# Kernel tuning notes

Measured on AMD Instinct MI355X. Metric: run time of the kernel, lower is better.

The kernel has to match this reference:

```python
import jax, jax.numpy as jnp
import numpy as np

EMBED_DIM = 1024
WINDOW = 256
NUM_HEADS = 16
HEAD_DIM = EMBED_DIM // NUM_HEADS
SCALE = HEAD_DIM ** (-0.5)


def setup_inputs() -> dict:
    key = jax.random.key(0)
    ks = jax.random.split(key, 9)
    B, S, E = 4, 4096, EMBED_DIM
    std = E ** (-0.5)
    x = jax.random.normal(ks[0], (B, S, E), dtype=jnp.float32)
    Wq = jax.random.normal(ks[1], (E, E), dtype=jnp.float32) * std
    Wk = jax.random.normal(ks[2], (E, E), dtype=jnp.float32) * std
    Wv = jax.random.normal(ks[3], (E, E), dtype=jnp.float32) * std
    Wo = jax.random.normal(ks[4], (E, E), dtype=jnp.float32) * std
    bq = jax.random.normal(ks[5], (E,), dtype=jnp.float32) * 0.01
    bk = jax.random.normal(ks[6], (E,), dtype=jnp.float32) * 0.01
    bv = jax.random.normal(ks[7], (E,), dtype=jnp.float32) * 0.01
    bo = jax.random.normal(ks[8], (E,), dtype=jnp.float32) * 0.01
    return {"x": x, "Wq": Wq, "bq": bq, "Wk": Wk, "bk": bk,
            "Wv": Wv, "bv": bv, "Wo": Wo, "bo": bo}


def reference(x, Wq, bq, Wk, bk, Wv, bv, Wo, bo):
    B, S, E = x.shape
    W = WINDOW
    nw = S // W  # seq_len chosen divisible by window_size
    # projections (torch Linear: x @ W.T + b); no head split in the original
    q = x @ Wq.T + bq
    k = x @ Wk.T + bk
    v = x @ Wv.T + bv
    # split into non-overlapping windows: [B, nw, W, E]
    qw = q.reshape(B, nw, W, E)
    kw = k.reshape(B, nw, W, E)
    vw = v.reshape(B, nw, W, E)
    scores = jnp.einsum('bnqe,bnke->bnqk', qw, kw) * SCALE  # [B, nw, W, W]
    causal = jnp.tril(jnp.ones((W, W), dtype=bool))
    scores = jnp.where(causal, scores, -jnp.inf)
    attn = jax.nn.softmax(scores, axis=-1)
    out = jnp.einsum('bnqk,bnke->bnqe', attn, vw).reshape(B, S, E)
    out = out @ Wo.T + bo
    return out + x
```

## Files before the change

kernel.cpp:

```cpp
#include <hip/hip_runtime.h>
#include <hip/hip_bf16.h>


typedef unsigned short u16;
typedef __attribute__((ext_vector_type(8))) short short8;
typedef __attribute__((ext_vector_type(4))) float f32x4;

__device__ __forceinline__ u16 f2bf(float f) {
    __hip_bfloat16 h = __float2bfloat16(f);
    return __builtin_bit_cast(u16, h);
}

__global__ void cast_x(const float* __restrict__ x, u16* __restrict__ xb, u16* __restrict__ xt) {
    __shared__ float lt[64][65];
    const int t = threadIdx.x;
    const int e0 = blockIdx.x * 64, i0 = blockIdx.y * 64;
    const int tr = t >> 3, tc = (t & 7) * 8;
#pragma unroll
    for (int p = 0; p < 2; ++p) {
        int r = p * 32 + tr;
        const float* s = x + (size_t)(i0 + r) * 1024 + e0 + tc;
        float4 a = *(const float4*)s, b = *(const float4*)(s + 4);
        short8 o;
        o[0] = (short)f2bf(a.x); o[1] = (short)f2bf(a.y); o[2] = (short)f2bf(a.z); o[3] = (short)f2bf(a.w);
        o[4] = (short)f2bf(b.x); o[5] = (short)f2bf(b.y); o[6] = (short)f2bf(b.z); o[7] = (short)f2bf(b.w);
        *(short8*)(xb + (size_t)(i0 + r) * 1024 + e0 + tc) = o;
        lt[r][tc + 0] = a.x; lt[r][tc + 1] = a.y; lt[r][tc + 2] = a.z; lt[r][tc + 3] = a.w;
        lt[r][tc + 4] = b.x; lt[r][tc + 5] = b.y; lt[r][tc + 6] = b.z; lt[r][tc + 7] = b.w;
    }
    __syncthreads();
#pragma unroll
    for (int p = 0; p < 2; ++p) {
        int r = p * 32 + tr;
        short8 o;
#pragma unroll
        for (int j = 0; j < 8; ++j) o[j] = (short)f2bf(lt[tc + j][r]);
        *(short8*)(xt + (size_t)(e0 + r) * 16384 + i0 + tc) = o;
    }
}

__global__ void wcast(const float* __restrict__ Wq, const float* __restrict__ Wk,
                      const float* __restrict__ Wv, const float* __restrict__ Wo,
                      u16* __restrict__ WqT, u16* __restrict__ WkT,
                      u16* __restrict__ WvT, u16* __restrict__ Wob)
{
    __shared__ float lt[64][65];
    const int which = blockIdx.x >> 8;
    const int bid = blockIdx.x & 255;
    const int c0 = (bid & 15) * 64, r0 = (bid >> 4) * 64;
    const int t = threadIdx.x;
    const int tr = t >> 3, tc = (t & 7) * 8;
    const float* src = which == 0 ? Wq : which == 1 ? Wk : which == 2 ? Wv : Wo;
    if (which == 3) {
#pragma unroll
        for (int p = 0; p < 2; ++p) {
            int r = p * 32 + tr;
            const float* s = src + (size_t)(r0 + r) * 1024 + c0 + tc;
            float4 a = *(const float4*)s, b = *(const float4*)(s + 4);
            short8 o;
            o[0] = (short)f2bf(a.x); o[1] = (short)f2bf(a.y); o[2] = (short)f2bf(a.z); o[3] = (short)f2bf(a.w);
            o[4] = (short)f2bf(b.x); o[5] = (short)f2bf(b.y); o[6] = (short)f2bf(b.z); o[7] = (short)f2bf(b.w);
            *(short8*)(Wob + (size_t)(r0 + r) * 1024 + c0 + tc) = o;
        }
        return;
    }
    u16* dst = which == 0 ? WqT : which == 1 ? WkT : WvT;
#pragma unroll
    for (int p = 0; p < 2; ++p) {
        int r = p * 32 + tr;
        const float* s = src + (size_t)(r0 + r) * 1024 + c0 + tc;
        float4 a = *(const float4*)s, b = *(const float4*)(s + 4);
        lt[r][tc + 0] = a.x; lt[r][tc + 1] = a.y; lt[r][tc + 2] = a.z; lt[r][tc + 3] = a.w;
        lt[r][tc + 4] = b.x; lt[r][tc + 5] = b.y; lt[r][tc + 6] = b.z; lt[r][tc + 7] = b.w;
    }
    __syncthreads();
#pragma unroll
    for (int p = 0; p < 2; ++p) {
        int r = p * 32 + tr;
        short8 o;
#pragma unroll
        for (int j = 0; j < 8; ++j) o[j] = (short)f2bf(lt[tc + j][r]);
        *(short8*)(dst + (size_t)(c0 + r) * 1024 + r0 + tc) = o;
    }
}

__global__ void ub2(const float* __restrict__ Wk, const float* __restrict__ bq,
                    const float* __restrict__ Wo, const float* __restrict__ bv,
                    const float* __restrict__ bo, float* __restrict__ u, float* __restrict__ b2)
{
    const int t = threadIdx.x, bid = blockIdx.x;
    if (bid < 4) {
        int b = bid * 256 + t;
        float acc = 0.f;
        for (int o = 0; o < 1024; ++o) acc += Wk[(size_t)o * 1024 + b] * bq[o];
        u[b] = acc;
    } else {
        int n = (bid - 4) * 16 + (t >> 4);
        int l = t & 15;
        float acc = 0.f;
        for (int m = l; m < 1024; m += 16) acc += Wo[(size_t)n * 1024 + m] * bv[m];
#pragma unroll
        for (int s = 1; s < 16; s <<= 1) acc += __shfl_xor(acc, s, 64);
        if (l == 0) b2[n] = acc + bo[n];
    }
}

__global__ __launch_bounds__(256, 4) void gemm_small_dual(
    const u16* __restrict__ HA, const u16* __restrict__ HB, u16* __restrict__ HC,
    const u16* __restrict__ WA, const u16* __restrict__ WB, u16* __restrict__ WC)
{
    __shared__ __align__(16) u16 At[64 * 64], Bt[64 * 64];
    const bool sec = blockIdx.x >= 256;
    const u16* A = sec ? WA : HA;
    const u16* B = sec ? WB : HB;
    u16* C = sec ? WC : HC;
    const int bid = blockIdx.x & 255;
    const int m0 = (bid >> 4) * 64, n0 = (bid & 15) * 64;
    const int t = threadIdx.x, lane = t & 63, w = t >> 6;
    const int l15 = lane & 15, lk = lane >> 4;

    f32x4 acc[4];
#pragma unroll
    for (int m = 0; m < 4; ++m) acc[m] = (f32x4){0.f, 0.f, 0.f, 0.f};

    for (int k0 = 0; k0 < 1024; k0 += 64) {
        __syncthreads();
#pragma unroll
        for (int p = 0; p < 2; ++p) {
            int e = p * 2048 + t * 8;
            int row = e >> 6, col = e & 63;
            short8 va = *(const short8*)(A + (size_t)(m0 + row) * 1024 + k0 + col);
            *(short8*)((char*)At + row * 128 + ((col * 2) ^ ((row & 7) << 4))) = va;
            short8 vb = *(const short8*)(B + (size_t)(n0 + row) * 1024 + k0 + col);
            *(short8*)((char*)Bt + row * 128 + ((col * 2) ^ ((row & 7) << 4))) = vb;
        }
        __syncthreads();
#pragma unroll
        for (int ks = 0; ks < 2; ++ks) {
            int bc = ks * 64 + lk * 16;
            int brow = w * 16 + l15;
            short8 bfr = *(const short8*)((char*)Bt + brow * 128 + (bc ^ ((brow & 7) << 4)));
#pragma unroll
            for (int m = 0; m < 4; ++m) {
                int arow = m * 16 + l15;
                short8 af = *(const short8*)((char*)At + arow * 128 + (bc ^ ((arow & 7) << 4)));
                acc[m] = __builtin_amdgcn_mfma_f32_16x16x32_bf16(af, bfr, acc[m], 0, 0, 0);
            }
        }
    }
#pragma unroll
    for (int m = 0; m < 4; ++m)
#pragma unroll
        for (int r = 0; r < 4; ++r) {
            int row = m0 + m * 16 + lk * 4 + r;
            int col = n0 + w * 16 + l15;
            C[(size_t)row * 1024 + col] = f2bf(acc[m][r]);
        }
}

template <int EPI>
__global__ __launch_bounds__(256, 2) void gemm_bt(
    const u16* __restrict__ A, const u16* __restrict__ B,
    int M, int N, int K,
    const float* __restrict__ bias0,
    u16* __restrict__ Cb, float* __restrict__ Cf, const float* __restrict__ resid)
{
    __shared__ __align__(16) u16 At[128 * 64];
    __shared__ __align__(16) u16 Bt[128 * 64];
    const int t = threadIdx.x;
    const int lane = t & 63;
    const int wid = t >> 6;
    const int wm = wid >> 1, wn = wid & 1;
    const int l15 = lane & 15, lk = lane >> 4;

    const int bid = blockIdx.y * gridDim.x + blockIdx.x;
    const int nwg = gridDim.x * gridDim.y;
    const int cpx = nwg >> 3;
    const int swz = (bid & 7) * cpx + (bid >> 3);
    const int tn = swz & 7;
    const int tm = swz >> 3;
    const int m0 = tm * 128, n0 = tn * 128;

    f32x4 acc[4][4];
#pragma unroll
    for (int m = 0; m < 4; ++m)
#pragma unroll
        for (int n = 0; n < 4; ++n)
            acc[m][n] = (f32x4){0.f, 0.f, 0.f, 0.f};

    for (int k0 = 0; k0 < K; k0 += 64) {
        __syncthreads();
#pragma unroll
        for (int p = 0; p < 4; ++p) {
            int e = p * 2048 + t * 8;
            int row = e >> 6, col = e & 63;
            short8 va = *(const short8*)(A + (size_t)(m0 + row) * K + k0 + col);
            *(short8*)((char*)At + row * 128 + ((col * 2) ^ ((row & 7) << 4))) = va;
            short8 vb = *(const short8*)(B + (size_t)(n0 + row) * K + k0 + col);
            *(short8*)((char*)Bt + row * 128 + ((col * 2) ^ ((row & 7) << 4))) = vb;
        }
        __syncthreads();
#pragma unroll
        for (int ks = 0; ks < 2; ++ks) {
            const int bc = ks * 64 + lk * 16;
            short8 af[4], bfr[4];
#pragma unroll
            for (int m = 0; m < 4; ++m) {
                int row = wm * 64 + m * 16 + l15;
                af[m] = *(const short8*)((char*)At + row * 128 + (bc ^ ((row & 7) << 4)));
            }
#pragma unroll
            for (int n = 0; n < 4; ++n) {
                int row = wn * 64 + n * 16 + l15;
                bfr[n] = *(const short8*)((char*)Bt + row * 128 + (bc ^ ((row & 7) << 4)));
            }
#pragma unroll
            for (int m = 0; m < 4; ++m)
#pragma unroll
                for (int n = 0; n < 4; ++n)
                    acc[m][n] = __builtin_amdgcn_mfma_f32_16x16x32_bf16(af[m], bfr[n], acc[m][n], 0, 0, 0);
        }
    }

#pragma unroll
    for (int m = 0; m < 4; ++m) {
#pragma unroll
        for (int n = 0; n < 4; ++n) {
            int col = n0 + wn * 64 + n * 16 + l15;
            float bv = bias0[col];
#pragma unroll
            for (int r = 0; r < 4; ++r) {
                int row = m0 + wm * 64 + m * 16 + lk * 4 + r;
                float v = acc[m][n][r] + bv;
                if (EPI == 0)
                    Cb[(size_t)row * N + col] = f2bf(v);
                else
                    Cf[(size_t)row * N + col] = v + resid[(size_t)row * N + col];
            }
        }
    }
}

__global__ __launch_bounds__(256, 1) void attn_win(
    const u16* __restrict__ y, const u16* __restrict__ xb,
    const u16* __restrict__ xt, u16* __restrict__ z)
{
    __shared__ __align__(16) char smem[100608];
    float* S = (float*)smem;
    u16* P = (u16*)(smem + 65792);
    float* rmax = (float*)(smem + 98560);
    float* rsum = (float*)(smem + 99584);
    u16* Qt = (u16*)smem;
    u16* Kt = (u16*)(smem + 8192);
    u16* Vl = (u16*)smem;

    const int t = threadIdx.x;
    const int lane = t & 63, wv = t >> 6;
    const int l15 = lane & 15, lk = lane >> 4;
    const int bid = blockIdx.x;
    const int swz = (bid & 7) * 32 + (bid >> 3);
    const int win = swz >> 2, qc = swz & 3;
    const size_t qrow0 = (size_t)win * 256 + qc * 64;
    const size_t krow0 = (size_t)win * 256;

    f32x4 acc[4][4];
#pragma unroll
    for (int m = 0; m < 4; ++m)
#pragma unroll
        for (int n = 0; n < 4; ++n)
            acc[m][n] = (f32x4){0.f, 0.f, 0.f, 0.f};

    for (int e0 = 0; e0 < 1024; e0 += 64) {
        __syncthreads();
#pragma unroll
        for (int p = 0; p < 2; ++p) {
            int e = p * 2048 + t * 8;
            int row = e >> 6, col = e & 63;
            short8 v = *(const short8*)(y + (qrow0 + row) * 1024 + e0 + col);
            *(short8*)((char*)Qt + row * 128 + ((col * 2) ^ ((row & 7) << 4))) = v;
        }
#pragma unroll
        for (int p = 0; p < 8; ++p) {
            int e = p * 2048 + t * 8;
            int row = e >> 6, col = e & 63;
            short8 v = *(const short8*)(xb + (krow0 + row) * 1024 + e0 + col);
            *(short8*)((char*)Kt + row * 128 + ((col * 2) ^ ((row & 7) << 4))) = v;
        }
        __syncthreads();
#pragma unroll
        for (int ks = 0; ks < 2; ++ks) {
            const int bc = ks * 64 + lk * 16;
            short8 af[4], bfr[4];
#pragma unroll
            for (int m = 0; m < 4; ++m) {
                int row = m * 16 + l15;
                af[m] = *(const short8*)((char*)Qt + row * 128 + (bc ^ ((row & 7) << 4)));
            }
#pragma unroll
            for (int n = 0; n < 4; ++n) {
                int row = wv * 64 + n * 16 + l15;
                bfr[n] = *(const short8*)((char*)Kt + row * 128 + (bc ^ ((row & 7) << 4)));
            }
#pragma unroll
            for (int m = 0; m < 4; ++m)
#pragma unroll
                for (int n = 0; n < 4; ++n)
                    acc[m][n] = __builtin_amdgcn_mfma_f32_16x16x32_bf16(af[m], bfr[n], acc[m][n], 0, 0, 0);
        }
    }
    __syncthreads();

#pragma unroll
    for (int m = 0; m < 4; ++m) {
#pragma unroll
        for (int n = 0; n < 4; ++n) {
            int col = wv * 64 + n * 16 + l15;
#pragma unroll
            for (int r = 0; r < 4; ++r) {
                int row = m * 16 + lk * 4 + r;
                int qpos = qc * 64 + row;
                float v = acc[m][n][r] * 0.125f;
                S[row * 257 + col] = (col <= qpos) ? v : -1e30f;
            }
        }
    }
    __syncthreads();
    {
        const int row = t & 63, q4 = t >> 6;
        float* Sr = S + row * 257 + q4 * 64;
        float lmax = -1e30f;
        for (int i = 0; i < 64; ++i) lmax = fmaxf(lmax, Sr[i]);
        rmax[row * 4 + q4] = lmax;
        __syncthreads();
        float m4 = fmaxf(fmaxf(rmax[row * 4], rmax[row * 4 + 1]),
                         fmaxf(rmax[row * 4 + 2], rmax[row * 4 + 3]));
        float lsum = 0.f;
        for (int i = 0; i < 64; ++i) {
            float e = __expf(Sr[i] - m4);
            Sr[i] = e;
            lsum += e;
        }
        rsum[row * 4 + q4] = lsum;
        __syncthreads();
        float inv = 1.f / (rsum[row * 4] + rsum[row * 4 + 1] + rsum[row * 4 + 2] + rsum[row * 4 + 3]);
#pragma unroll
        for (int i8 = 0; i8 < 8; ++i8) {
            short8 pv;
#pragma unroll
            for (int j = 0; j < 8; ++j) pv[j] = (short)f2bf(Sr[i8 * 8 + j] * inv);
            int col = q4 * 64 + i8 * 8;
            *(short8*)((char*)P + row * 512 + ((col * 2) ^ ((row & 7) << 4))) = pv;
        }
    }

    for (int n0 = 0; n0 < 1024; n0 += 64) {
        __syncthreads();
#pragma unroll
        for (int p = 0; p < 8; ++p) {
            int e = p * 2048 + t * 8;
            int row = e >> 8, col = e & 255;
            short8 v = *(const short8*)(xt + (size_t)(n0 + row) * 16384 + win * 256 + col);
            *(short8*)((char*)Vl + row * 512 + ((col * 2) ^ ((row & 7) << 4))) = v;
        }
        __syncthreads();
        f32x4 acc2[4];
#pragma unroll
        for (int m = 0; m < 4; ++m) acc2[m] = (f32x4){0.f, 0.f, 0.f, 0.f};
#pragma unroll
        for (int ks = 0; ks < 8; ++ks) {
            const int bc = ks * 64 + lk * 16;
            short8 af[4];
#pragma unroll
            for (int m = 0; m < 4; ++m) {
                int row = m * 16 + l15;
                af[m] = *(const short8*)((char*)P + row * 512 + (bc ^ ((row & 7) << 4)));
            }
            int vrow = wv * 16 + l15;
            short8 bfr = *(const short8*)((char*)Vl + vrow * 512 + (bc ^ ((vrow & 7) << 4)));
#pragma unroll
            for (int m = 0; m < 4; ++m)
                acc2[m] = __builtin_amdgcn_mfma_f32_16x16x32_bf16(af[m], bfr, acc2[m], 0, 0, 0);
        }
#pragma unroll
        for (int m = 0; m < 4; ++m) {
#pragma unroll
            for (int r = 0; r < 4; ++r) {
                int row = m * 16 + lk * 4 + r;
                int col = n0 + wv * 16 + l15;
                z[(qrow0 + row) * 1024 + col] = f2bf(acc2[m][r]);
            }
        }
    }
}

extern "C" void kernel_launch(void* const* d_in, const int* in_sizes, int n_in,
                              void* d_out, int out_size, void* d_ws, size_t ws_size,
                              hipStream_t stream) {
    const float* x  = (const float*)d_in[0];
    const float* Wq = (const float*)d_in[1];
    const float* bq = (const float*)d_in[2];
    const float* Wk = (const float*)d_in[3];
    const float* Wv = (const float*)d_in[5];
    const float* bv = (const float*)d_in[6];
    const float* Wo = (const float*)d_in[7];
    const float* bo = (const float*)d_in[8];
    float* out = (float*)d_out;

    char* ws = (char*)d_ws;
    u16* xb  = (u16*)(ws);
    u16* xt  = (u16*)(ws + 33554432);
    u16* yb  = (u16*)(ws + 67108864);
    u16* zb  = (u16*)(ws + 100663296);
    u16* WqT = (u16*)(ws + 134217728);
    u16* WkT = (u16*)(ws + 136314880);
    u16* WvT = (u16*)(ws + 138412032);
    u16* Wob = (u16*)(ws + 140509184);
    u16* Hb  = (u16*)(ws + 142606336);
    u16* W2b = (u16*)(ws + 144703488);
    float* u_  = (float*)(ws + 146800640);
    float* b2_ = (float*)(ws + 146804736);

    cast_x<<<dim3(16, 256), 256, 0, stream>>>(x, xb, xt);
    wcast<<<1024, 256, 0, stream>>>(Wq, Wk, Wv, Wo, WqT, WkT, WvT, Wob);
    ub2<<<68, 256, 0, stream>>>(Wk, bq, Wo, bv, bo, u_, b2_);
    gemm_small_dual<<<512, 256, 0, stream>>>(WkT, WqT, Hb, Wob, WvT, W2b);
    gemm_bt<0><<<dim3(8, 128), 256, 0, stream>>>(xb, Hb, 16384, 1024, 1024, u_, yb, nullptr, nullptr);
    attn_win<<<256, 256, 0, stream>>>(yb, xb, xt, zb);
    gemm_bt<1><<<dim3(8, 128), 256, 0, stream>>>(zb, W2b, 16384, 1024, 1024, b2_, nullptr, out, x);
}
```

Baseline: 221.2 us.

## Register-prefetch GEMM tiles, register-resident softmax, and two blocks per CU for attention

The GEMM now prefetches the next K-tile of A and B into registers while the current tile is computed, which hides global load latency. The attention kernel drops the fp32 S score buffer in shared memory. Softmax now runs on the MFMA accumulators using wave shuffles plus small per-wave max and sum arrays. That cuts shared memory from about 100KB to 75KB, so launch bounds can allow two blocks per CU. s_setprio is also placed around the MFMA bursts, and P is now written with scalar 16-bit stores, which may cost some LDS store efficiency.

```diff
diff --git a/kernel.cpp b/kernel.cpp
--- a/kernel.cpp
+++ b/kernel.cpp
@@ -181,6 +181,8 @@
     const int tm = swz >> 3;
     const int m0 = tm * 128, n0 = tn * 128;
 
+    const int srow = (t * 8) >> 6, scol = (t * 8) & 63;
+
     f32x4 acc[4][4];
 #pragma unroll
     for (int m = 0; m < 4; ++m)
@@ -188,18 +190,29 @@
         for (int n = 0; n < 4; ++n)
             acc[m][n] = (f32x4){0.f, 0.f, 0.f, 0.f};
 
+    short8 pva[4], pvb[4];
+#pragma unroll
+    for (int p = 0; p < 4; ++p) {
+        pva[p] = *(const short8*)(A + (size_t)(m0 + p * 32 + srow) * K + scol);
+        pvb[p] = *(const short8*)(B + (size_t)(n0 + p * 32 + srow) * K + scol);
+    }
+
     for (int k0 = 0; k0 < K; k0 += 64) {
         __syncthreads();
 #pragma unroll
         for (int p = 0; p < 4; ++p) {
-            int e = p * 2048 + t * 8;
-            int row = e >> 6, col = e & 63;
-            short8 va = *(const short8*)(A + (size_t)(m0 + row) * K + k0 + col);
-            *(short8*)((char*)At + row * 128 + ((col * 2) ^ ((row & 7) << 4))) = va;
-            short8 vb = *(const short8*)(B + (size_t)(n0 + row) * K + k0 + col);
-            *(short8*)((char*)Bt + row * 128 + ((col * 2) ^ ((row & 7) << 4))) = vb;
-        }
-        __syncthreads();
+            int row = p * 32 + srow;
+            *(short8*)((char*)At + row * 128 + ((scol * 2) ^ ((row & 7) << 4))) = pva[p];
+            *(short8*)((char*)Bt + row * 128 + ((scol * 2) ^ ((row & 7) << 4))) = pvb[p];
+        }
+        __syncthreads();
+        if (k0 + 64 < K) {
+#pragma unroll
+            for (int p = 0; p < 4; ++p) {
+                pva[p] = *(const short8*)(A + (size_t)(m0 + p * 32 + srow) * K + k0 + 64 + scol);
+                pvb[p] = *(const short8*)(B + (size_t)(n0 + p * 32 + srow) * K + k0 + 64 + scol);
+            }
+        }
 #pragma unroll
         for (int ks = 0; ks < 2; ++ks) {
             const int bc = ks * 64 + lk * 16;
@@ -241,18 +254,17 @@
     }
 }
 
-__global__ __launch_bounds__(256, 1) void attn_win(
+__global__ __launch_bounds__(256, 2) void attn_win(
     const u16* __restrict__ y, const u16* __restrict__ xb,
     const u16* __restrict__ xt, u16* __restrict__ z)
 {
-    __shared__ __align__(16) char smem[100608];
-    float* S = (float*)smem;
-    u16* P = (u16*)(smem + 65792);
-    float* rmax = (float*)(smem + 98560);
-    float* rsum = (float*)(smem + 99584);
+    __shared__ __align__(16) char smem[75776];
     u16* Qt = (u16*)smem;
     u16* Kt = (u16*)(smem + 8192);
     u16* Vl = (u16*)smem;
+    u16* P  = (u16*)(smem + 40960);
+    float* rmax = (float*)(smem + 73728);
+    float* rsum = (float*)(smem + 74752);
 
     const int t = threadIdx.x;
     const int lane = t & 63, wv = t >> 6;
@@ -301,57 +313,73 @@
                 int row = wv * 64 + n * 16 + l15;
                 bfr[n] = *(const short8*)((char*)Kt + row * 128 + (bc ^ ((row & 7) << 4)));
             }
+            __builtin_amdgcn_s_setprio(1);
 #pragma unroll
             for (int m = 0; m < 4; ++m)
 #pragma unroll
                 for (int n = 0; n < 4; ++n)
                     acc[m][n] = __builtin_amdgcn_mfma_f32_16x16x32_bf16(af[m], bfr[n], acc[m][n], 0, 0, 0);
-        }
-    }
-    __syncthreads();
-
-#pragma unroll
-    for (int m = 0; m < 4; ++m) {
+            __builtin_amdgcn_s_setprio(0);
+        }
+    }
+
+#pragma unroll
+    for (int m = 0; m < 4; ++m)
 #pragma unroll
         for (int n = 0; n < 4; ++n) {
             int col = wv * 64 + n * 16 + l15;
 #pragma unroll
             for (int r = 0; r < 4; ++r) {
-                int row = m * 16 + lk * 4 + r;
-                int qpos = qc * 64 + row;
+                int qpos = qc * 64 + m * 16 + lk * 4 + r;
                 float v = acc[m][n][r] * 0.125f;
-                S[row * 257 + col] = (col <= qpos) ? v : -1e30f;
-            }
-        }
-    }
+                acc[m][n][r] = (col <= qpos) ? v : -1e30f;
+            }
+        }
+#pragma unroll
+    for (int m = 0; m < 4; ++m)
+#pragma unroll
+        for (int r = 0; r < 4; ++r) {
+            float tmx = fmaxf(fmaxf(acc[m][0][r], acc[m][1][r]), fmaxf(acc[m][2][r], acc[m][3][r]));
+            tmx = fmaxf(tmx, __shfl_xor(tmx, 1));
+            tmx = fmaxf(tmx, __shfl_xor(tmx, 2));
+            tmx = fmaxf(tmx, __shfl_xor(tmx, 4));
+            tmx = fmaxf(tmx, __shfl_xor(tmx, 8));
+            if (l15 == 0) rmax[(m * 16 + lk * 4 + r) * 4 + wv] = tmx;
+        }
     __syncthreads();
-    {
-        const int row = t & 63, q4 = t >> 6;
-        float* Sr = S + row * 257 + q4 * 64;
-        float lmax = -1e30f;
-        for (int i = 0; i < 64; ++i) lmax = fmaxf(lmax, Sr[i]);
-        rmax[row * 4 + q4] = lmax;
-        __syncthreads();
-        float m4 = fmaxf(fmaxf(rmax[row * 4], rmax[row * 4 + 1]),
-                         fmaxf(rmax[row * 4 + 2], rmax[row * 4 + 3]));
-        float lsum = 0.f;
-        for (int i = 0; i < 64; ++i) {
-            float e = __expf(Sr[i] - m4);
-            Sr[i] = e;
-            lsum += e;
-        }
-        rsum[row * 4 + q4] = lsum;
-        __syncthreads();
-        float inv = 1.f / (rsum[row * 4] + rsum[row * 4 + 1] + rsum[row * 4 + 2] + rsum[row * 4 + 3]);
-#pragma unroll
-        for (int i8 = 0; i8 < 8; ++i8) {
-            short8 pv;
-#pragma unroll
-            for (int j = 0; j < 8; ++j) pv[j] = (short)f2bf(Sr[i8 * 8 + j] * inv);
-            int col = q4 * 64 + i8 * 8;
-            *(short8*)((char*)P + row * 512 + ((col * 2) ^ ((row & 7) << 4))) = pv;
-        }
-    }
+#pragma unroll
+    for (int m = 0; m < 4; ++m)
+#pragma unroll
+        for (int r = 0; r < 4; ++r) {
+            int row = m * 16 + lk * 4 + r;
+            float m4 = fmaxf(fmaxf(rmax[row * 4], rmax[row * 4 + 1]),
+                             fmaxf(rmax[row * 4 + 2], rmax[row * 4 + 3]));
+            float s = 0.f;
+#pragma unroll
+            for (int n = 0; n < 4; ++n) {
+                float e = __expf(acc[m][n][r] - m4);
+                acc[m][n][r] = e;
+                s += e;
+            }
+            s += __shfl_xor(s, 1);
+            s += __shfl_xor(s, 2);
+            s += __shfl_xor(s, 4);
+            s += __shfl_xor(s, 8);
+            if (l15 == 0) rsum[row * 4 + wv] = s;
+        }
+    __syncthreads();
+#pragma unroll
+    for (int m = 0; m < 4; ++m)
+#pragma unroll
+        for (int r = 0; r < 4; ++r) {
+            int row = m * 16 + lk * 4 + r;
+            float inv = 1.f / (rsum[row * 4] + rsum[row * 4 + 1] + rsum[row * 4 + 2] + rsum[row * 4 + 3]);
+#pragma unroll
+            for (int n = 0; n < 4; ++n) {
+                int col = wv * 64 + n * 16 + l15;
+                *(u16*)((char*)P + row * 512 + ((col * 2) ^ ((row & 7) << 4))) = f2bf(acc[m][n][r] * inv);
+            }
+        }
 
     for (int n0 = 0; n0 < 1024; n0 += 64) {
         __syncthreads();
@@ -377,9 +405,11 @@
             }
             int vrow = wv * 16 + l15;
             short8 bfr = *(const short8*)((char*)Vl + vrow * 512 + (bc ^ ((vrow & 7) << 4)));
+            __builtin_amdgcn_s_setprio(1);
 #pragma unroll
             for (int m = 0; m < 4; ++m)
                 acc2[m] = __builtin_amdgcn_mfma_f32_16x16x32_bf16(af[m], bfr, acc2[m], 0, 0, 0);
+            __builtin_amdgcn_s_setprio(0);
         }
 #pragma unroll
         for (int m = 0; m < 4; ++m) {
```

Measured after the change: 223.4 us. About the same (+1.0%).
